# Optimization experiments

Hardware: AMD Instinct MI355X
Metric: run time of the kernel (lower is better)

The kernel has to match this reference:

```python
import jax, jax.numpy as jnp
import numpy as np

F_DIM, H, B, MAX = 128, 256, 256, 128
N = B * MAX            # 32768 nodes, 256 graphs of 128 nodes each
E = 524288             # avg degree 16
EPS = 1e-5


def _bn(x, g, b):
    # BatchNorm1d in training mode: biased batch stats over the node axis
    m = x.mean(0)
    v = x.var(0)
    return (x - m) * jax.lax.rsqrt(v + EPS) * g + b


def _gcn(x, W, b, src, dst, n):
    # PyG GCNConv: add self-loops, symmetric deg^-1/2 normalization
    h = x @ W
    loops = jnp.arange(n, dtype=src.dtype)
    s = jnp.concatenate([src, loops])
    d = jnp.concatenate([dst, loops])
    deg = jax.ops.segment_sum(jnp.ones_like(s, dtype=x.dtype), d, num_segments=n)
    dinv = jax.lax.rsqrt(jnp.maximum(deg, 1.0))
    norm = dinv[s] * dinv[d]
    out = jax.ops.segment_sum(h[s] * norm[:, None], d, num_segments=n)
    return out + b


def setup_inputs() -> dict:
    key = jax.random.key(0)
    ks = jax.random.split(key, 20)

    def xavier(k, shape, gain=1.414):
        lim = gain * np.sqrt(6.0 / (shape[0] + shape[1]))
        return jax.random.uniform(k, shape, jnp.float32, -lim, lim)

    inp = {}
    inp['x'] = jax.random.normal(ks[0], (N, F_DIM), jnp.float32)
    inp['src_local'] = jax.random.randint(ks[1], (E,), 0, MAX, jnp.int32)
    inp['dst_local'] = jax.random.randint(ks[2], (E,), 0, MAX, jnp.int32)
    dims = [(F_DIM, H), (H, H), (H, H)]
    for i, (di, do) in enumerate(dims):
        inp[f'gcn_w{i}'] = xavier(ks[3 + i], (di, do))
        inp[f'gcn_b{i}'] = jnp.zeros((do,), jnp.float32)
        inp[f'bn_g{i}'] = jnp.ones((do,), jnp.float32)
        inp[f'bn_b{i}'] = jnp.zeros((do,), jnp.float32)
    inp['sc_w0'] = xavier(ks[6], (F_DIM, H), 1.0)
    inp['sc_b0'] = jnp.zeros((H,), jnp.float32)
    inp['edge_w'] = xavier(ks[7], (H, H), 0.01)
    inp['fd_w0'] = xavier(ks[8], (H, H)); inp['fd_b0'] = jnp.zeros((H,), jnp.float32)
    inp['fd_g0'] = jnp.ones((H,), jnp.float32); inp['fd_be0'] = jnp.zeros((H,), jnp.float32)
    inp['fd_w1'] = xavier(ks[9], (H, H)); inp['fd_b1'] = jnp.zeros((H,), jnp.float32)
    inp['fd_g1'] = jnp.ones((H,), jnp.float32); inp['fd_be1'] = jnp.zeros((H,), jnp.float32)
    inp['fd_w2'] = xavier(ks[10], (H, F_DIM)); inp['fd_b2'] = jnp.zeros((F_DIM,), jnp.float32)
    inp['ph_w0'] = xavier(ks[11], (H, H)); inp['ph_b0'] = jnp.zeros((H,), jnp.float32)
    inp['ph_w1'] = xavier(ks[12], (H, H)); inp['ph_b1'] = jnp.zeros((H,), jnp.float32)
    return inp


def reference(x, src_local, dst_local,
              gcn_w0, gcn_b0, bn_g0, bn_b0, sc_w0, sc_b0,
              gcn_w1, gcn_b1, bn_g1, bn_b1,
              gcn_w2, gcn_b2, bn_g2, bn_b2,
              edge_w,
              fd_w0, fd_b0, fd_g0, fd_be0,
              fd_w1, fd_b1, fd_g1, fd_be1,
              fd_w2, fd_b2,
              ph_w0, ph_b0, ph_w1, ph_b1):
    n = x.shape[0]
    # global edge index: edge e belongs to graph e // (E//B); offset by g*MAX
    off = (jnp.arange(E, dtype=jnp.int32) // (E // B)) * MAX
    src = src_local + off
    dst = dst_local + off

    def block(h, W, b, g, bb, shortcut):
        res = shortcut(h)
        out = jax.nn.relu(_bn(_gcn(h, W, b, src, dst, n), g, bb))
        return jax.nn.relu(out + res)  # dropout is identity at inference

    z = block(x, gcn_w0, gcn_b0, bn_g0, bn_b0, lambda h: h @ sc_w0 + sc_b0)
    z = block(z, gcn_w1, gcn_b1, bn_g1, bn_b1, lambda h: h)
    z = block(z, gcn_w2, gcn_b2, bn_g2, bn_b2, lambda h: h)
    # F.normalize(p=2, dim=1)
    z = z / jnp.maximum(jnp.linalg.norm(z, axis=1, keepdims=True), 1e-12)

    # BilinearEdgeDecoder per graph, vectorized: sigmoid(Z W Z^T) with zero diag
    zb = z.reshape(B, MAX, H)
    adj = jax.nn.sigmoid(jnp.einsum('bnd,de,bme->bnm', zb, edge_w, zb))
    adj = adj * (1.0 - jnp.eye(MAX, dtype=adj.dtype))

    # Feature_Decoder: [Linear,ReLU,BN] x2 then Linear
    h = _bn(jax.nn.relu(z @ fd_w0 + fd_b0), fd_g0, fd_be0)
    h = _bn(jax.nn.relu(h @ fd_w1 + fd_b1), fd_g1, fd_be1)
    x_recon = h @ fd_w2 + fd_b2

    z_g = zb.max(axis=1)  # global_max_pool per graph
    z_g_mlp = jax.nn.relu(z_g @ ph_w0 + ph_b0) @ ph_w1 + ph_b1
    return (z, adj, x_recon, z_g, z_g_mlp)
```

## Files before the change

kernel.cpp:

```cpp
#include <hip/hip_runtime.h>
#include <hip/hip_bf16.h>

using bf = __hip_bfloat16;
typedef __attribute__((ext_vector_type(8))) short s8;
typedef __attribute__((ext_vector_type(4))) float f4;

constexpr int NN  = 32768;
constexpr int HD  = 256;

__device__ __forceinline__ float u2f(unsigned short h) {
    union { unsigned u; float f; } x; x.u = ((unsigned)h) << 16;
    return x.f;
}
__device__ __forceinline__ unsigned short f2u(float f) {
    union { float f; unsigned u; } x; x.f = f;
    unsigned r = x.u + 0x7FFF + ((x.u >> 16) & 1);
    return (unsigned short)(r >> 16);
}
__device__ __forceinline__ bf f2bf(float f) {
    unsigned short h = f2u(f);
    return *reinterpret_cast<bf*>(&h);
}
__device__ __forceinline__ float bf2f(bf b) {
    return u2f(*reinterpret_cast<unsigned short*>(&b));
}

__device__ __forceinline__ int swz(int row, int slot) {
    return row * 64 + ((slot ^ (row & 7)) << 3);
}
__device__ __forceinline__ int swz128(int row, int slot) {
    return row * 128 + ((slot ^ (row & 7)) << 3);
}

typedef const __attribute__((address_space(1))) unsigned int guint;
typedef __attribute__((address_space(3))) unsigned int luint;
__device__ __forceinline__ void gload16(const void* g, void* l) {
    __builtin_amdgcn_global_load_lds((guint*)g, (luint*)l, 16, 0, 0);
}

struct WTd { const float* src; int K, N, off; };
struct WTpack { WTd w[10]; };

__global__ __launch_bounds__(256) void k_prep(const int* __restrict__ srcL,
                                              const int* __restrict__ dstL,
                                              const float* __restrict__ xf,
                                              WTpack p, bf* __restrict__ A,
                                              bf* __restrict__ xb,
                                              bf* __restrict__ wT) {
    __shared__ __align__(16) float shm[8320];
    int b = blockIdx.x, t = threadIdx.x;
    if (b < 256) {
        float* sT = shm;
        float* sdin = shm + 8192;
        int g = b;
        const int* sg = srcL + (g << 11);
        const int* dg = dstL + (g << 11);
        if (t < 128) sdin[t] = 0.f;
        __syncthreads();
        for (int e = t; e < 2048; e += 256) atomicAdd(&sdin[dg[e]], 1.0f);
        __syncthreads();
        if (t < 128) sdin[t] = rsqrtf(sdin[t] + 1.0f);
        __syncthreads();
        bf* out = A + ((long)g << 14);
        for (int half = 0; half < 2; ++half) {
            for (int i = t; i < 8192; i += 256) sT[i] = 0.f;
            __syncthreads();
            for (int e = t; e < 2048; e += 256) {
                int s = sg[e], d = dg[e];
                if ((s >> 6) == half)
                    atomicAdd(&sT[(d << 6) + (s & 63)], sdin[s] * sdin[d]);
            }
            __syncthreads();
            if (t < 128 && (t >> 6) == half)
                sT[(t << 6) + (t & 63)] += sdin[t] * sdin[t];
            __syncthreads();
            for (int i4 = t; i4 < 2048; i4 += 256) {
                int d = i4 >> 4, c4 = (i4 & 15) * 4;
                float4 v = *(float4*)&sT[(d << 6) + c4];
                ushort4 u = make_ushort4(f2u(v.x), f2u(v.y), f2u(v.z), f2u(v.w));
                *(ushort4*)&out[(d << 7) + (half << 6) + c4] = u;
            }
            __syncthreads();
        }
    } else if (b < 416) {
        int idx = b - 256;
        WTd d = p.w[idx >> 4];
        int rem = idx & 15;
        int n0 = (rem & 3) * 64, k0 = (rem >> 2) * 64;
        if (n0 >= d.N || k0 >= d.K) return;
        float (*s)[65] = (float(*)[65])shm;
        int cc = t & 63, rq = t >> 6;
#pragma unroll
        for (int i = 0; i < 16; ++i) {
            int r = i * 4 + rq;
            s[r][cc] = d.src[(long)(k0 + r) * d.N + n0 + cc];
        }
        __syncthreads();
#pragma unroll
        for (int i = 0; i < 16; ++i) {
            int r = i * 4 + rq;
            wT[d.off + (long)(n0 + r) * d.K + k0 + cc] = f2bf(s[cc][r]);
        }
    } else {
        long base = (long)(b - 416) * 16384;
#pragma unroll
        for (int it = 0; it < 16; ++it) {
            long i4 = base + (it * 256 + t) * 4;
            float4 v = *(const float4*)&xf[i4];
            *(ushort4*)&xb[i4] = make_ushort4(f2u(v.x), f2u(v.y), f2u(v.z), f2u(v.w));
        }
    }
}

__device__ __forceinline__ void mfma_s1(const bf* sA, const bf* sB, f4 (&acc)[4][2],
                                        int wm, int wn, int l15, int kq) {
#pragma unroll
    for (int ks = 0; ks < 2; ++ks) {
        s8 af[4], bg[2];
#pragma unroll
        for (int f = 0; f < 4; ++f)
            af[f] = *(const s8*)&sA[swz(wm * 64 + f * 16 + l15, kq + 4 * ks)];
#pragma unroll
        for (int f = 0; f < 2; ++f)
            bg[f] = *(const s8*)&sB[swz(wn * 32 + f * 16 + l15, kq + 4 * ks)];
#pragma unroll
        for (int fr = 0; fr < 4; ++fr)
#pragma unroll
            for (int fc = 0; fc < 2; ++fc)
                acc[fr][fc] = __builtin_amdgcn_mfma_f32_16x16x32_bf16(
                    af[fr], bg[fc], acc[fr][fc], 0, 0, 0);
    }
}

__device__ __forceinline__ void mfma_s2(const bf* sA, const bf* sB, f4 (&acc)[4][2],
                                        int wm, int wn, int l15, int kq) {
#pragma unroll
    for (int ks = 0; ks < 4; ++ks) {
        s8 af[4], bg[2];
#pragma unroll
        for (int f = 0; f < 4; ++f)
            af[f] = *(const s8*)&sA[swz128(wm * 64 + f * 16 + l15, ks * 4 + kq)];
#pragma unroll
        for (int f = 0; f < 2; ++f)
            bg[f] = *(const s8*)&sB[swz128(wn * 32 + f * 16 + l15, ks * 4 + kq)];
#pragma unroll
        for (int fr = 0; fr < 4; ++fr)
#pragma unroll
            for (int fc = 0; fc < 2; ++fc)
                acc[fr][fc] = __builtin_amdgcn_mfma_f32_16x16x32_bf16(
                    af[fr], bg[fc], acc[fr][fc], 0, 0, 0);
    }
}

__device__ __forceinline__ void tstore(bf* sOut, f4 (&acc)[4][2],
                                       int wm, int wn, int l15, int kq) {
#pragma unroll
    for (int fr = 0; fr < 4; ++fr) {
        int rl = wm * 64 + fr * 16 + kq * 4;
#pragma unroll
        for (int fc = 0; fc < 2; ++fc) {
            int cl = wn * 32 + fc * 16 + l15;
            ushort4 q = make_ushort4(f2u(acc[fr][fc][0]), f2u(acc[fr][fc][1]),
                                     f2u(acc[fr][fc][2]), f2u(acc[fr][fc][3]));
            int off = cl * 128 + (((rl >> 3) ^ (cl & 7)) << 3) + (rl & 7);
            *(ushort4*)&sOut[off] = q;
        }
    }
}

template <int MODE>
__global__ __launch_bounds__(512) void k_fused(
    const bf* __restrict__ Xin,
    const bf* __restrict__ Res, const float* __restrict__ stats,
    const bf* __restrict__ Wt, const bf* __restrict__ Wt2,
    const float* __restrict__ scb, const bf* __restrict__ Adj,
    bf* __restrict__ Zout, bf* __restrict__ AG, bf* __restrict__ ResOut,
    float* __restrict__ part) {
    __shared__ __align__(16) bf sOut[16384];
    __shared__ __align__(16) bf sStg[16384];
    const int g = blockIdx.x;
    const int h = blockIdx.y;
    const int t = threadIdx.x;
    const int lane = t & 63, w = t >> 6;
    const int wm = w >> 2, wn = w & 3;
    const int l15 = lane & 15, kq = lane >> 4;
    constexpr int KS1 = (MODE == 2) ? 128 : 256;
    const bf* Xg = Xin + (long)g * ((MODE == 2) ? 16384 : 32768);
    const bf* Rg = (MODE == 0) ? Res + (long)g * 32768 : nullptr;

    f4 acc1[4][2] = {};
    for (int k0 = 0; k0 < KS1; k0 += 64) {
        __syncthreads();
#pragma unroll
        for (int i = 0; i < 2; ++i) {
            if constexpr (MODE == 0) {
                int sdx = i * 512 + t;
                int row = sdx >> 3, sl = sdx & 7;
                int c = k0 + sl * 8;
                s8 av = *(const s8*)&Xg[row * 256 + c];
                s8 rv = *(const s8*)&Rg[row * 256 + c];
                float4 sc0 = *(const float4*)&stats[c];
                float4 sc1 = *(const float4*)&stats[c + 4];
                float4 sh0 = *(const float4*)&stats[256 + c];
                float4 sh1 = *(const float4*)&stats[256 + c + 4];
                float scv[8] = {sc0.x, sc0.y, sc0.z, sc0.w, sc1.x, sc1.y, sc1.z, sc1.w};
                float shv[8] = {sh0.x, sh0.y, sh0.z, sh0.w, sh1.x, sh1.y, sh1.z, sh1.w};
                unsigned short* u = (unsigned short*)&av;
                const unsigned short* ru = (const unsigned short*)&rv;
#pragma unroll
                for (int j = 0; j < 8; ++j) {
                    float v = fmaf(u2f(u[j]), scv[j], shv[j]);
                    v = fmaxf(v, 0.f) + u2f(ru[j]);
                    u[j] = f2u(fmaxf(v, 0.f));
                }
                if (h == 0)
                    *(s8*)&Zout[(long)g * 32768 + row * 256 + c] = av;
                *(s8*)&sStg[swz(row, sl)] = av;
            } else {
                int r0 = i * 64 + 8 * w;
                int rw = r0 + (lane >> 3);
                int ps = ((lane & 7) ^ (rw & 7)) << 3;
                gload16(&Xg[rw * 128 + k0 + ps], &sStg[r0 * 64]);
            }
            {
                int r0 = i * 64 + 8 * w;
                int rw = r0 + (lane >> 3);
                int ps = ((lane & 7) ^ (rw & 7)) << 3;
                const bf* bsrc;
                if constexpr (MODE == 0)
                    bsrc = &Wt[(h * 128 + rw) * 256 + k0 + ps];
                else {
                    const bf* Wsrc = (h < 2) ? Wt : Wt2;
                    bsrc = &Wsrc[((h & 1) * 128 + rw) * 128 + k0 + ps];
                }
                gload16(bsrc, &sStg[8192 + r0 * 64]);
            }
        }
        __syncthreads();
        mfma_s1(sStg, sStg + 8192, acc1, wm, wn, l15, kq);
    }
    if (MODE == 2 && h >= 2) {
#pragma unroll
        for (int fr = 0; fr < 4; ++fr) {
            int rl = wm * 64 + fr * 16 + kq * 4;
#pragma unroll
            for (int fc = 0; fc < 2; ++fc) {
                int cl = wn * 32 + fc * 16 + l15;
                float bv = scb[(h - 2) * 128 + cl];
#pragma unroll
                for (int i = 0; i < 4; ++i)
                    ResOut[(long)(g * 128 + rl + i) * 256 + (h - 2) * 128 + cl] =
                        f2bf(acc1[fr][fc][i] + bv);
            }
        }
        return;
    }
    tstore(sOut, acc1, wm, wn, l15, kq);
    __syncthreads();
#pragma unroll
    for (int i = 0; i < 4; ++i) {
        int r0 = i * 32 + 4 * w;
        int rw = r0 + (lane >> 4);
        int ps = ((lane & 15) ^ (rw & 7)) << 3;
        gload16(&Adj[((long)g << 14) + rw * 128 + ps], &sStg[r0 * 128]);
    }
    __syncthreads();
    f4 acc2[4][2] = {};
    mfma_s2(sStg, sOut, acc2, wm, wn, l15, kq);
    float ps[2] = {0.f, 0.f}, ps2[2] = {0.f, 0.f};
#pragma unroll
    for (int fr = 0; fr < 4; ++fr) {
        int rl = wm * 64 + fr * 16 + kq * 4;
#pragma unroll
        for (int fc = 0; fc < 2; ++fc) {
            int cl = wn * 32 + fc * 16 + l15;
#pragma unroll
            for (int i = 0; i < 4; ++i) {
                float v = acc2[fr][fc][i];
                ps[fc] += v; ps2[fc] += v * v;
                AG[(long)(g * 128 + rl + i) * 256 + (h & 1) * 128 + cl] = f2bf(v);
            }
        }
    }
    __syncthreads();
    float* scr = (float*)sStg;
#pragma unroll
    for (int fc = 0; fc < 2; ++fc) {
        ps[fc] += __shfl_xor(ps[fc], 16);  ps[fc] += __shfl_xor(ps[fc], 32);
        ps2[fc] += __shfl_xor(ps2[fc], 16); ps2[fc] += __shfl_xor(ps2[fc], 32);
    }
    if (lane < 16) {
#pragma unroll
        for (int fc = 0; fc < 2; ++fc) {
            int c = wn * 32 + fc * 16 + lane;
            scr[(c * 2 + wm) * 2 + 0] = ps[fc];
            scr[(c * 2 + wm) * 2 + 1] = ps2[fc];
        }
    }
    __syncthreads();
    if (t < 256) {
        int col = t & 127, s = t >> 7;
        part[(long)((h & 1) * 256 + g) * 256 + s * 128 + col] =
            scr[(col * 2 + 0) * 2 + s] + scr[(col * 2 + 1) * 2 + s];
    }
}

__device__ __forceinline__ void fd_layer(const bf* Zg, const bf* W, const float* bias,
                                         bf* C, float* part, bf* sStg,
                                         int g, int h, int t, int lane,
                                         int wm, int wn, int l15, int kq) {
    f4 acc[4][2] = {};
    for (int k0 = 0; k0 < 256; k0 += 64) {
        __syncthreads();
#pragma unroll
        for (int i = 0; i < 2; ++i) {
            int sdx = i * 512 + t;
            int row = sdx >> 3, sl = sdx & 7;
            int c = k0 + sl * 8;
            *(s8*)&sStg[swz(row, sl)] = *(const s8*)&Zg[row * 256 + c];
            *(s8*)&sStg[8192 + swz(row, sl)] = *(const s8*)&W[(h * 128 + row) * 256 + c];
        }
        __syncthreads();
        mfma_s1(sStg, sStg + 8192, acc, wm, wn, l15, kq);
    }
    float ps[2] = {0.f, 0.f}, ps2[2] = {0.f, 0.f};
#pragma unroll
    for (int fr = 0; fr < 4; ++fr) {
        int rl = wm * 64 + fr * 16 + kq * 4;
#pragma unroll
        for (int fc = 0; fc < 2; ++fc) {
            int cl = wn * 32 + fc * 16 + l15;
            float bv = bias[h * 128 + cl];
#pragma unroll
            for (int i = 0; i < 4; ++i) {
                float v = fmaxf(acc[fr][fc][i] + bv, 0.f);
                ps[fc] += v; ps2[fc] += v * v;
                C[(long)(g * 128 + rl + i) * 256 + h * 128 + cl] = f2bf(v);
            }
        }
    }
    __syncthreads();
    float* scr = (float*)sStg;
#pragma unroll
    for (int fc = 0; fc < 2; ++fc) {
        ps[fc] += __shfl_xor(ps[fc], 16);  ps[fc] += __shfl_xor(ps[fc], 32);
        ps2[fc] += __shfl_xor(ps2[fc], 16); ps2[fc] += __shfl_xor(ps2[fc], 32);
    }
    if (lane < 16) {
#pragma unroll
        for (int fc = 0; fc < 2; ++fc) {
            int c = wn * 32 + fc * 16 + lane;
            scr[(c * 2 + wm) * 2 + 0] = ps[fc];
            scr[(c * 2 + wm) * 2 + 1] = ps2[fc];
        }
    }
    __syncthreads();
    if (t < 256) {
        int col = t & 127, s = t >> 7;
        part[(long)(h * 256 + g) * 256 + s * 128 + col] =
            scr[(col * 2 + 0) * 2 + s] + scr[(col * 2 + 1) * 2 + s];
    }
}

__global__ __launch_bounds__(512) void k_edfd(
    const bf* __restrict__ Zn, const bf* __restrict__ ewT,
    const bf* __restrict__ fdw, const float* __restrict__ fdb,
    float* __restrict__ adjout, bf* __restrict__ C, float* __restrict__ part) {
    __shared__ __align__(16) bf sOut[16384];
    __shared__ __align__(16) bf sStg[16384];
    const int t = threadIdx.x;
    const int lane = t & 63, w = t >> 6;
    const int wm = w >> 2, wn = w & 3;
    const int l15 = lane & 15, kq = lane >> 4;
    if (blockIdx.x >= 256) {
        int bb = blockIdx.x - 256;
        int g = bb & 255, h = bb >> 8;
        fd_layer(Zn + (long)g * 32768, fdw, fdb, C, part, sStg,
                 g, h, t, lane, wm, wn, l15, kq);
        return;
    }
    const int g = blockIdx.x;
    const bf* Xg = Zn + (long)g * 32768;
    f4 acc2[4][2] = {};
    for (int h = 0; h < 2; ++h) {
        f4 acc1[4][2] = {};
        for (int k0 = 0; k0 < 256; k0 += 64) {
            __syncthreads();
#pragma unroll
            for (int i = 0; i < 2; ++i) {
                int sdx = i * 512 + t;
                int row = sdx >> 3, sl = sdx & 7;
                int c = k0 + sl * 8;
                *(s8*)&sStg[swz(row, sl)] = *(const s8*)&ewT[(h * 128 + row) * 256 + c];
                *(s8*)&sStg[8192 + swz(row, sl)] = *(const s8*)&Xg[row * 256 + c];
            }
            __syncthreads();
            mfma_s1(sStg, sStg + 8192, acc1, wm, wn, l15, kq);
        }
        tstore(sOut, acc1, wm, wn, l15, kq);
        __syncthreads();
#pragma unroll
        for (int i = 0; i < 4; ++i) {
            int sdx = i * 512 + t;
            int row = sdx >> 4, sl = sdx & 15;
            *(s8*)&sStg[swz128(row, sl)] = *(const s8*)&Xg[row * 256 + h * 128 + sl * 8];
        }
        __syncthreads();
        mfma_s2(sStg, sOut, acc2, wm, wn, l15, kq);
        __syncthreads();
    }
#pragma unroll
    for (int fr = 0; fr < 4; ++fr) {
        int rl = wm * 64 + fr * 16 + kq * 4;
#pragma unroll
        for (int fc = 0; fc < 2; ++fc) {
            int cl = wn * 32 + fc * 16 + l15;
            float vv[4];
#pragma unroll
            for (int i = 0; i < 4; ++i) {
                float v = 1.f / (1.f + __expf(-acc2[fr][fc][i]));
                if (cl == rl + i) v = 0.f;
                vv[i] = v;
            }
            float4 o; o.x = vv[0]; o.y = vv[1]; o.z = vv[2]; o.w = vv[3];
            *(float4*)&adjout[((long)g << 14) + cl * 128 + rl] = o;
        }
    }
}

template <int EPI, int OUT, bool PART, bool BNA, bool AF32>
__global__ __launch_bounds__(256) void mg(
    const void* __restrict__ Av, const bf* __restrict__ BT,
    const float* __restrict__ bias, const float* __restrict__ bnstats,
    float* __restrict__ Cf, bf* __restrict__ Cb, float* __restrict__ part,
    int M, int N, int K, int ldc) {
    __shared__ __align__(16) bf sAl[128 * 64];
    __shared__ __align__(16) bf sBl[128 * 64];
    const int m0 = blockIdx.y * 128, n0 = blockIdx.x * 128;
    const bf* Bb = BT + (long)n0 * K;
    const int t = threadIdx.x;
    const int lane = t & 63;
    const int w = t >> 6;
    const int wm = (w >> 1) * 64, wn = (w & 1) * 64;
    const int fr16 = lane & 15, kq = lane >> 4;
    f4 acc[4][4] = {};
    for (int k0 = 0; k0 < K; k0 += 64) {
#pragma unroll
        for (int i = 0; i < 4; ++i) {
            int sdx = i * 256 + t;
            int row = sdx >> 3, sl = sdx & 7;
            s8 av;
            if constexpr (AF32) {
                const float* src = (const float*)Av + (long)(m0 + row) * K + k0 + sl * 8;
                float4 f0 = *(const float4*)src;
                float4 f1 = *(const float4*)(src + 4);
                unsigned short u[8] = {f2u(f0.x), f2u(f0.y), f2u(f0.z), f2u(f0.w),
                                       f2u(f1.x), f2u(f1.y), f2u(f1.z), f2u(f1.w)};
                av = *(s8*)u;
            } else {
                av = *(const s8*)&((const bf*)Av)[(long)(m0 + row) * K + k0 + sl * 8];
                if constexpr (BNA) {
                    int c = k0 + sl * 8;
                    float4 sc0 = *(const float4*)&bnstats[c];
                    float4 sc1 = *(const float4*)&bnstats[c + 4];
                    float4 sh0 = *(const float4*)&bnstats[256 + c];
                    float4 sh1 = *(const float4*)&bnstats[256 + c + 4];
                    float scv[8] = {sc0.x, sc0.y, sc0.z, sc0.w, sc1.x, sc1.y, sc1.z, sc1.w};
                    float shv[8] = {sh0.x, sh0.y, sh0.z, sh0.w, sh1.x, sh1.y, sh1.z, sh1.w};
                    unsigned short* u = (unsigned short*)&av;
#pragma unroll
                    for (int j = 0; j < 8; ++j)
                        u[j] = f2u(fmaf(u2f(u[j]), scv[j], shv[j]));
                }
            }
            *(s8*)&sAl[swz(row, sl)] = av;
            *(s8*)&sBl[swz(row, sl)] = *(const s8*)&Bb[(long)row * K + k0 + sl * 8];
        }
        __syncthreads();
#pragma unroll
        for (int ks = 0; ks < 2; ++ks) {
            s8 af[4], bg[4];
#pragma unroll
            for (int f = 0; f < 4; ++f) {
                af[f] = *(const s8*)&sAl[swz(wm + f * 16 + fr16, kq + 4 * ks)];
                bg[f] = *(const s8*)&sBl[swz(wn + f * 16 + fr16, kq + 4 * ks)];
            }
#pragma unroll
            for (int fr = 0; fr < 4; ++fr)
#pragma unroll
                for (int fc = 0; fc < 4; ++fc)
                    acc[fr][fc] = __builtin_amdgcn_mfma_f32_16x16x32_bf16(
                        af[fr], bg[fc], acc[fr][fc], 0, 0, 0);
        }
        __syncthreads();
    }
    float ps[4], ps2[4];
    if (PART) {
#pragma unroll
        for (int fc = 0; fc < 4; ++fc) { ps[fc] = 0.f; ps2[fc] = 0.f; }
    }
#pragma unroll
    for (int fr = 0; fr < 4; ++fr) {
        int rl = wm + fr * 16 + (lane >> 4) * 4;
#pragma unroll
        for (int fc = 0; fc < 4; ++fc) {
            int cl = wn + fc * 16 + (lane & 15);
            int col = n0 + cl;
            float bv = bias[col];
#pragma unroll
            for (int i = 0; i < 4; ++i) {
                float v = acc[fr][fc][i] + bv;
                if (EPI == 2) v = fmaxf(v, 0.f);
                if (PART) { ps[fc] += v; ps2[fc] += v * v; }
                if (OUT == 0) Cf[(long)(m0 + rl + i) * ldc + col] = v;
                if (OUT == 1) Cb[(long)(m0 + rl + i) * ldc + col] = f2bf(v);
            }
        }
    }
    if (PART) {
        __syncthreads();
        float* scr = (float*)sAl;
#pragma unroll
        for (int fc = 0; fc < 4; ++fc) {
            ps[fc] += __shfl_xor(ps[fc], 16);  ps[fc] += __shfl_xor(ps[fc], 32);
            ps2[fc] += __shfl_xor(ps2[fc], 16); ps2[fc] += __shfl_xor(ps2[fc], 32);
        }
        if (lane < 16) {
#pragma unroll
            for (int fc = 0; fc < 4; ++fc) {
                scr[(w * 2 + 0) * 64 + fc * 16 + lane] = ps[fc];
                scr[(w * 2 + 1) * 64 + fc * 16 + lane] = ps2[fc];
            }
        }
        __syncthreads();
        int id = blockIdx.x * gridDim.y + blockIdx.y;
        int stat = t >> 7, c = t & 127;
        int ci = c & 63, half = c >> 6;
        float v = scr[(half * 2 + stat) * 64 + ci] + scr[((half + 2) * 2 + stat) * 64 + ci];
        part[(long)id * 256 + stat * 128 + c] = v;
    }
}

__global__ void k_bnfin(const float* __restrict__ part, const float* __restrict__ gam,
                        const float* __restrict__ bet, float* __restrict__ stats) {
    int ch = blockIdx.x;
    int half = ch >> 7, cc = ch & 127;
    int t = threadIdx.x;
    __shared__ float2 sm[256];
    const float* p = part + (long)(half * 256 + t) * 256;
    sm[t] = make_float2(p[cc], p[128 + cc]);
    __syncthreads();
    for (int s = 128; s > 0; s >>= 1) {
        if (t < s) { sm[t].x += sm[t + s].x; sm[t].y += sm[t + s].y; }
        __syncthreads();
    }
    if (t == 0) {
        float m = sm[0].x / (float)NN;
        float var = sm[0].y / (float)NN - m * m;
        float sc = rsqrtf(var + 1e-5f) * gam[ch];
        stats[ch]       = sc;
        stats[256 + ch] = bet[ch] - m * sc;
    }
}

__global__ __launch_bounds__(512) void k_finz(
    const bf* __restrict__ X, const float* __restrict__ stats,
    const bf* __restrict__ res, float* __restrict__ outz, bf* __restrict__ Znb,
    unsigned* __restrict__ zgu) {
    int g = blockIdx.x, half = blockIdx.y;
    int t = threadIdx.x;
    int lane = t & 63, w = t >> 6;
    int c4 = lane * 4;
    float4 sc = *(const float4*)&stats[c4];
    float4 sh = *(const float4*)&stats[256 + c4];
    float scv[4] = {sc.x, sc.y, sc.z, sc.w};
    float shv[4] = {sh.x, sh.y, sh.z, sh.w};
    float cmax[4] = {0.f, 0.f, 0.f, 0.f};
#pragma unroll
    for (int it = 0; it < 8; ++it) {
        int r = half * 64 + w * 8 + it;
        long i = (long)(g * 128 + r) * 256 + c4;
        ushort4 xv = *(const ushort4*)(X + i);
        ushort4 rv = *(const ushort4*)(res + i);
        unsigned short xs[4] = {xv.x, xv.y, xv.z, xv.w};
        unsigned short rs[4] = {rv.x, rv.y, rv.z, rv.w};
        float v[4];
        float s = 0.f;
#pragma unroll
        for (int j = 0; j < 4; ++j) {
            float vv = fmaf(u2f(xs[j]), scv[j], shv[j]);
            vv = fmaxf(vv, 0.f) + u2f(rs[j]);
            vv = fmaxf(vv, 0.f);
            v[j] = vv;
            s += vv * vv;
        }
#pragma unroll
        for (int o = 1; o < 64; o <<= 1) s += __shfl_xor(s, o);
        float den = fmaxf(sqrtf(s), 1e-12f);
        float4 fo;
        unsigned short us[4];
#pragma unroll
        for (int j = 0; j < 4; ++j) {
            float o = v[j] / den;
            ((float*)&fo)[j] = o;
            us[j] = f2u(o);
            cmax[j] = fmaxf(cmax[j], o);
        }
        *(float4*)(outz + i) = fo;
        *(ushort4*)(Znb + i) = make_ushort4(us[0], us[1], us[2], us[3]);
    }
    __shared__ float pm[8][256];
#pragma unroll
    for (int j = 0; j < 4; ++j) pm[w][c4 + j] = cmax[j];
    __syncthreads();
    if (t < 256) {
        float m = pm[0][t];
#pragma unroll
        for (int ww = 1; ww < 8; ++ww) m = fmaxf(m, pm[ww][t]);
        atomicMax(&zgu[g * 256 + t], __float_as_uint(m));
    }
}

template <int EPI, int OUT, bool PART, bool BNA, bool AF32>
static void MG(hipStream_t st, const void* A, const bf* BT, const float* bias,
               const float* bnstats, float* Cf, bf* Cb, float* part,
               int M, int N, int K, int ldc) {
    dim3 g(N / 128, M / 128, 1);
    mg<EPI, OUT, PART, BNA, AF32><<<g, 256, 0, st>>>(A, BT, bias, bnstats, Cf, Cb, part,
                                                     M, N, K, ldc);
}

extern "C" void kernel_launch(void* const* d_in, const int* in_sizes, int n_in,
                              void* d_out, int out_size, void* d_ws, size_t ws_size,
                              hipStream_t stream) {
    const float* x      = (const float*)d_in[0];
    const int*   srcL   = (const int*)d_in[1];
    const int*   dstL   = (const int*)d_in[2];
    const float* gcn_w0 = (const float*)d_in[3];
    const float* bn_g0  = (const float*)d_in[5];
    const float* bn_b0  = (const float*)d_in[6];
    const float* gcn_w1 = (const float*)d_in[7];
    const float* bn_g1  = (const float*)d_in[9];
    const float* bn_b1  = (const float*)d_in[10];
    const float* gcn_w2 = (const float*)d_in[11];
    const float* bn_g2  = (const float*)d_in[13];
    const float* bn_b2  = (const float*)d_in[14];
    const float* sc_w0  = (const float*)d_in[15];
    const float* sc_b0  = (const float*)d_in[16];
    const float* edge_w = (const float*)d_in[17];
    const float* fd_w0  = (const float*)d_in[18];
    const float* fd_b0  = (const float*)d_in[19];
    const float* fd_g0  = (const float*)d_in[20];
    const float* fd_be0 = (const float*)d_in[21];
    const float* fd_w1  = (const float*)d_in[22];
    const float* fd_b1  = (const float*)d_in[23];
    const float* fd_g1  = (const float*)d_in[24];
    const float* fd_be1 = (const float*)d_in[25];
    const float* fd_w2  = (const float*)d_in[26];
    const float* fd_b2  = (const float*)d_in[27];
    const float* ph_w0  = (const float*)d_in[28];
    const float* ph_b0  = (const float*)d_in[29];
    const float* ph_w1  = (const float*)d_in[30];
    const float* ph_b1  = (const float*)d_in[31];

    float* out     = (float*)d_out;
    float* out_z   = out;
    float* out_adj = out + 8388608;
    float* out_xr  = out + 12582912;
    float* out_zg  = out + 16777216;
    float* out_zgm = out + 16842752;

    float* w     = (float*)d_ws;
    float* part  = w;
    float* stats = w + 131072;
    bf*    wT    = (bf*)(w + 131584);
    bf*    Aadjb = (bf*)(w + 410112);
    bf*    U4    = (bf*)(w + 2507264);
    bf*    U1    = (bf*)(w + 6701568);
    bf*    U2    = (bf*)(w + 10895872);
    bf*    U3    = (bf*)(w + 15090176);
    bf*    P1b   = (bf*)(w + 19284480);
    bf*    xb    = (bf*)(w + 19317248);

    WTpack pk;
    pk.w[0] = {gcn_w0, 128, 256, 0};
    pk.w[1] = {sc_w0,  128, 256, 32768};
    pk.w[2] = {gcn_w1, 256, 256, 65536};
    pk.w[3] = {gcn_w2, 256, 256, 131072};
    pk.w[4] = {edge_w, 256, 256, 196608};
    pk.w[5] = {fd_w0,  256, 256, 262144};
    pk.w[6] = {fd_w1,  256, 256, 327680};
    pk.w[7] = {fd_w2,  256, 128, 393216};
    pk.w[8] = {ph_w0,  256, 256, 425984};
    pk.w[9] = {ph_w1,  256, 256, 491520};

    hipMemsetAsync(out_zg, 0, 65536 * 4, stream);

    k_prep<<<672, 256, 0, stream>>>(srcL, dstL, x, pk, Aadjb, xb, wT);

    k_fused<2><<<dim3(256, 4), 512, 0, stream>>>(xb, nullptr, nullptr,
                                                 wT + 0, wT + 32768, sc_b0, Aadjb,
                                                 nullptr, U2, U1, part);
    k_bnfin<<<256, 256, 0, stream>>>(part, bn_g0, bn_b0, stats);

    k_fused<0><<<dim3(256, 2), 512, 0, stream>>>(U2, U1, stats,
                                                 wT + 65536, nullptr, nullptr, Aadjb,
                                                 U3, U4, nullptr, part);
    k_bnfin<<<256, 256, 0, stream>>>(part, bn_g1, bn_b1, stats);

    k_fused<0><<<dim3(256, 2), 512, 0, stream>>>(U4, U3, stats,
                                                 wT + 131072, nullptr, nullptr, Aadjb,
                                                 U1, U2, nullptr, part);
    k_bnfin<<<256, 256, 0, stream>>>(part, bn_g2, bn_b2, stats);

    k_finz<<<dim3(256, 2), 512, 0, stream>>>(U2, stats, U1, out_z, U3,
                                             (unsigned*)out_zg);

    k_edfd<<<768, 512, 0, stream>>>(U3, wT + 196608, wT + 262144, fd_b0,
                                    out_adj, U4, part);
    k_bnfin<<<256, 256, 0, stream>>>(part, fd_g0, fd_be0, stats);

    MG<2, 1, true, true, false>(stream, U4, wT + 327680, fd_b1, stats,
                                nullptr, U2, part, NN, HD, HD, 256);
    k_bnfin<<<256, 256, 0, stream>>>(part, fd_g1, fd_be1, stats);
    MG<1, 0, false, true, false>(stream, U2, wT + 393216, fd_b2, stats,
                                 out_xr, nullptr, nullptr, NN, 128, HD, 128);

    MG<2, 1, false, false, true>(stream, out_zg, wT + 425984, ph_b0, nullptr,
                                 nullptr, P1b, nullptr, 256, 256, 256, 256);
    MG<1, 0, false, false, false>(stream, P1b, wT + 491520, ph_b1, nullptr,
                                  out_zgm, nullptr, nullptr, 256, 256, 256, 256);
}
```

Baseline: 182.8 us.

## Fuse GCN trunk layers, BN finalize and normalize into one cooperative kernel

Replaces the chain of three fused GCN kernels, three BN-finalize kernels and the final normalize/max-pool kernel with a single persistent cooperative kernel of 512 blocks. Grid-wide syncs separate the layers, and the BN statistics reduction is done inline by half the blocks. The aim is to remove several kernel launch gaps and tail effects. In exchange it adds grid-sync overhead. Each layer-0 block now runs the GCN and shortcut GEMMs back to back. Operand staging changes from direct global-to-LDS loads to loads through registers. A fallback path keeps the multi-kernel sequence in case the cooperative launch fails.

```diff
diff --git a/kernel.cpp b/kernel.cpp
--- a/kernel.cpp
+++ b/kernel.cpp
@@ -1,5 +1,8 @@
 #include <hip/hip_runtime.h>
 #include <hip/hip_bf16.h>
+#include <hip/hip_cooperative_groups.h>
+
+namespace cg = cooperative_groups;
 
 using bf = __hip_bfloat16;
 typedef __attribute__((ext_vector_type(8))) short s8;
@@ -30,12 +33,6 @@
 }
 __device__ __forceinline__ int swz128(int row, int slot) {
     return row * 128 + ((slot ^ (row & 7)) << 3);
-}
-
-typedef const __attribute__((address_space(1))) unsigned int guint;
-typedef __attribute__((address_space(3))) unsigned int luint;
-__device__ __forceinline__ void gload16(const void* g, void* l) {
-    __builtin_amdgcn_global_load_lds((guint*)g, (luint*)l, 16, 0, 0);
 }
 
 struct WTd { const float* src; int K, N, off; };
@@ -168,141 +165,355 @@
     }
 }
 
-template <int MODE>
-__global__ __launch_bounds__(512) void k_fused(
-    const bf* __restrict__ Xin,
-    const bf* __restrict__ Res, const float* __restrict__ stats,
-    const bf* __restrict__ Wt, const bf* __restrict__ Wt2,
-    const float* __restrict__ scb, const bf* __restrict__ Adj,
-    bf* __restrict__ Zout, bf* __restrict__ AG, bf* __restrict__ ResOut,
-    float* __restrict__ part) {
+__device__ __forceinline__ void stageAdj(bf* sStg, const bf* Adj, int g, int t) {
+#pragma unroll
+    for (int i = 0; i < 4; ++i) {
+        int sdx = i * 512 + t;
+        int row = sdx >> 4, sl = sdx & 15;
+        *(s8*)&sStg[swz128(row, sl)] =
+            *(const s8*)&Adj[((long)g << 14) + row * 128 + sl * 8];
+    }
+}
+
+__device__ __forceinline__ void ag_part(f4 (&acc2)[4][2], bf* AG, float* part,
+                                        bf* sStg, int g, int h, int t,
+                                        int wm, int wn, int l15, int kq, int lane) {
+    float ps[2] = {0.f, 0.f}, ps2[2] = {0.f, 0.f};
+#pragma unroll
+    for (int fr = 0; fr < 4; ++fr) {
+        int rl = wm * 64 + fr * 16 + kq * 4;
+#pragma unroll
+        for (int fc = 0; fc < 2; ++fc) {
+            int cl = wn * 32 + fc * 16 + l15;
+#pragma unroll
+            for (int i = 0; i < 4; ++i) {
+                float v = acc2[fr][fc][i];
+                ps[fc] += v; ps2[fc] += v * v;
+                AG[(long)(g * 128 + rl + i) * 256 + h * 128 + cl] = f2bf(v);
+            }
+        }
+    }
+    __syncthreads();
+    float* scr = (float*)sStg;
+#pragma unroll
+    for (int fc = 0; fc < 2; ++fc) {
+        ps[fc] += __shfl_xor(ps[fc], 16);  ps[fc] += __shfl_xor(ps[fc], 32);
+        ps2[fc] += __shfl_xor(ps2[fc], 16); ps2[fc] += __shfl_xor(ps2[fc], 32);
+    }
+    if (lane < 16) {
+#pragma unroll
+        for (int fc = 0; fc < 2; ++fc) {
+            int c = wn * 32 + fc * 16 + lane;
+            scr[(c * 2 + wm) * 2 + 0] = ps[fc];
+            scr[(c * 2 + wm) * 2 + 1] = ps2[fc];
+        }
+    }
+    __syncthreads();
+    if (t < 256) {
+        int col = t & 127, s = t >> 7;
+        part[(long)(h * 256 + g) * 256 + s * 128 + col] =
+            scr[(col * 2 + 0) * 2 + s] + scr[(col * 2 + 1) * 2 + s];
+    }
+}
+
+__device__ __forceinline__ void gcn_layer(const bf* Xg, const bf* Rg,
+                                          const float* stats, const bf* W,
+                                          const bf* Adj, bf* Zout, bf* AG,
+                                          float* part, bf* sOut, bf* sStg,
+                                          int g, int h, int t, int lane,
+                                          int wm, int wn, int l15, int kq) {
+    f4 acc1[4][2] = {};
+    for (int k0 = 0; k0 < 256; k0 += 64) {
+        __syncthreads();
+#pragma unroll
+        for (int i = 0; i < 2; ++i) {
+            int sdx = i * 512 + t;
+            int row = sdx >> 3, sl = sdx & 7;
+            int c = k0 + sl * 8;
+            s8 av = *(const s8*)&Xg[row * 256 + c];
+            s8 rv = *(const s8*)&Rg[row * 256 + c];
+            float4 sc0 = *(const float4*)&stats[c];
+            float4 sc1 = *(const float4*)&stats[c + 4];
+            float4 sh0 = *(const float4*)&stats[256 + c];
+            float4 sh1 = *(const float4*)&stats[256 + c + 4];
+            float scv[8] = {sc0.x, sc0.y, sc0.z, sc0.w, sc1.x, sc1.y, sc1.z, sc1.w};
+            float shv[8] = {sh0.x, sh0.y, sh0.z, sh0.w, sh1.x, sh1.y, sh1.z, sh1.w};
+            unsigned short* u = (unsigned short*)&av;
+            const unsigned short* ru = (const unsigned short*)&rv;
+#pragma unroll
+            for (int j = 0; j < 8; ++j) {
+                float v = fmaf(u2f(u[j]), scv[j], shv[j]);
+                v = fmaxf(v, 0.f) + u2f(ru[j]);
+                u[j] = f2u(fmaxf(v, 0.f));
+            }
+            if (Zout) *(s8*)&Zout[(long)g * 32768 + row * 256 + c] = av;
+            *(s8*)&sStg[swz(row, sl)] = av;
+            *(s8*)&sStg[8192 + swz(row, sl)] = *(const s8*)&W[(h * 128 + row) * 256 + c];
+        }
+        __syncthreads();
+        mfma_s1(sStg, sStg + 8192, acc1, wm, wn, l15, kq);
+    }
+    tstore(sOut, acc1, wm, wn, l15, kq);
+    __syncthreads();
+    stageAdj(sStg, Adj, g, t);
+    __syncthreads();
+    f4 acc2[4][2] = {};
+    mfma_s2(sStg, sOut, acc2, wm, wn, l15, kq);
+    ag_part(acc2, AG, part, sStg, g, h, t, wm, wn, l15, kq, lane);
+}
+
+__device__ __forceinline__ void l0_gcn(const bf* Xg, const bf* W0, const bf* Adj,
+                                       bf* AG, float* part, bf* sOut, bf* sStg,
+                                       int g, int h, int t, int lane,
+                                       int wm, int wn, int l15, int kq) {
+    f4 acc1[4][2] = {};
+    for (int k0 = 0; k0 < 128; k0 += 64) {
+        __syncthreads();
+#pragma unroll
+        for (int i = 0; i < 2; ++i) {
+            int sdx = i * 512 + t;
+            int row = sdx >> 3, sl = sdx & 7;
+            int c = k0 + sl * 8;
+            *(s8*)&sStg[swz(row, sl)] = *(const s8*)&Xg[row * 128 + c];
+            *(s8*)&sStg[8192 + swz(row, sl)] = *(const s8*)&W0[(h * 128 + row) * 128 + c];
+        }
+        __syncthreads();
+        mfma_s1(sStg, sStg + 8192, acc1, wm, wn, l15, kq);
+    }
+    tstore(sOut, acc1, wm, wn, l15, kq);
+    __syncthreads();
+    stageAdj(sStg, Adj, g, t);
+    __syncthreads();
+    f4 acc2[4][2] = {};
+    mfma_s2(sStg, sOut, acc2, wm, wn, l15, kq);
+    ag_part(acc2, AG, part, sStg, g, h, t, wm, wn, l15, kq, lane);
+}
+
+__device__ __forceinline__ void l0_sc(const bf* Xg, const bf* Wsc, const float* scb,
+                                      bf* ResOut, bf* sStg, int g, int h, int t,
+                                      int wm, int wn, int l15, int kq) {
+    f4 acc1[4][2] = {};
+    for (int k0 = 0; k0 < 128; k0 += 64) {
+        __syncthreads();
+#pragma unroll
+        for (int i = 0; i < 2; ++i) {
+            int sdx = i * 512 + t;
+            int row = sdx >> 3, sl = sdx & 7;
+            int c = k0 + sl * 8;
+            *(s8*)&sStg[swz(row, sl)] = *(const s8*)&Xg[row * 128 + c];
+            *(s8*)&sStg[8192 + swz(row, sl)] = *(const s8*)&Wsc[(h * 128 + row) * 128 + c];
+        }
+        __syncthreads();
+        mfma_s1(sStg, sStg + 8192, acc1, wm, wn, l15, kq);
+    }
+#pragma unroll
+    for (int fr = 0; fr < 4; ++fr) {
+        int rl = wm * 64 + fr * 16 + kq * 4;
+#pragma unroll
+        for (int fc = 0; fc < 2; ++fc) {
+            int cl = wn * 32 + fc * 16 + l15;
+            float bv = scb[h * 128 + cl];
+#pragma unroll
+            for (int i = 0; i < 4; ++i)
+                ResOut[(long)(g * 128 + rl + i) * 256 + h * 128 + cl] =
+                    f2bf(acc1[fr][fc][i] + bv);
+        }
+    }
+}
+
+__device__ __forceinline__ void bnfin_inline(const float* part, const float* gam,
+                                             const float* bet, float* stats,
+                                             void* lds, int ch, int t) {
+    float2* sm = (float2*)lds;
+    int half = ch >> 7, cc = ch & 127;
+    if (t < 256) {
+        const float* p = part + (long)(half * 256 + t) * 256;
+        sm[t] = make_float2(p[cc], p[128 + cc]);
+    }
+    __syncthreads();
+    for (int s = 128; s > 0; s >>= 1) {
+        if (t < s) { sm[t].x += sm[t + s].x; sm[t].y += sm[t + s].y; }
+        __syncthreads();
+    }
+    if (t == 0) {
+        float m = sm[0].x / (float)NN;
+        float var = sm[0].y / (float)NN - m * m;
+        float sc = rsqrtf(var + 1e-5f) * gam[ch];
+        stats[ch]       = sc;
+        stats[256 + ch] = bet[ch] - m * sc;
+    }
+}
+
+__device__ __forceinline__ void finz_inline(const bf* X, const float* stats,
+                                            const bf* res, float* outz, bf* Znb,
+                                            unsigned* zgu, float* pmLds,
+                                            int g, int half, int t) {
+    int lane = t & 63, w = t >> 6;
+    int c4 = lane * 4;
+    float4 sc = *(const float4*)&stats[c4];
+    float4 sh = *(const float4*)&stats[256 + c4];
+    float scv[4] = {sc.x, sc.y, sc.z, sc.w};
+    float shv[4] = {sh.x, sh.y, sh.z, sh.w};
+    float cmax[4] = {0.f, 0.f, 0.f, 0.f};
+#pragma unroll
+    for (int it = 0; it < 8; ++it) {
+        int r = half * 64 + w * 8 + it;
+        long i = (long)(g * 128 + r) * 256 + c4;
+        ushort4 xv = *(const ushort4*)(X + i);
+        ushort4 rv = *(const ushort4*)(res + i);
+        unsigned short xs[4] = {xv.x, xv.y, xv.z, xv.w};
+        unsigned short rs[4] = {rv.x, rv.y, rv.z, rv.w};
+        float v[4];
+        float s = 0.f;
+#pragma unroll
+        for (int j = 0; j < 4; ++j) {
+            float vv = fmaf(u2f(xs[j]), scv[j], shv[j]);
+            vv = fmaxf(vv, 0.f) + u2f(rs[j]);
+            vv = fmaxf(vv, 0.f);
+            v[j] = vv;
+            s += vv * vv;
+        }
+#pragma unroll
+        for (int o = 1; o < 64; o <<= 1) s += __shfl_xor(s, o);
+        float den = fmaxf(sqrtf(s), 1e-12f);
+        float4 fo;
+        unsigned short us[4];
+#pragma unroll
+        for (int j = 0; j < 4; ++j) {
+            float o = v[j] / den;
+            ((float*)&fo)[j] = o;
+            us[j] = f2u(o);
+            cmax[j] = fmaxf(cmax[j], o);
+        }
+        *(float4*)(outz + i) = fo;
+        *(ushort4*)(Znb + i) = make_ushort4(us[0], us[1], us[2], us[3]);
+    }
+    float (*pm)[256] = (float(*)[256])pmLds;
+    __syncthreads();
+#pragma unroll
+    for (int j = 0; j < 4; ++j) pm[w][c4 + j] = cmax[j];
+    __syncthreads();
+    if (t < 256) {
+        float m = pm[0][t];
+#pragma unroll
+        for (int ww = 1; ww < 8; ++ww) m = fmaxf(m, pm[ww][t]);
+        atomicMax(&zgu[g * 256 + t], __float_as_uint(m));
+    }
+}
+
+struct TrunkArgs {
+    const bf* xb; const bf* Adj; const bf* wT;
+    const float* scb;
+    const float* g0; const float* be0;
+    const float* g1; const float* be1;
+    const float* g2; const float* be2;
+    bf* U1; bf* U2; bf* U3; bf* U4;
+    float* part; float* stats;
+    float* outz; unsigned* zgu;
+};
+
+__global__ __launch_bounds__(512, 4) void k_trunk(TrunkArgs a) {
     __shared__ __align__(16) bf sOut[16384];
     __shared__ __align__(16) bf sStg[16384];
-    const int g = blockIdx.x;
-    const int h = blockIdx.y;
+    cg::grid_group gg = cg::this_grid();
+    const int b = blockIdx.x;
+    const int g = b & 255, hs = b >> 8;
     const int t = threadIdx.x;
     const int lane = t & 63, w = t >> 6;
     const int wm = w >> 2, wn = w & 3;
     const int l15 = lane & 15, kq = lane >> 4;
-    constexpr int KS1 = (MODE == 2) ? 128 : 256;
-    const bf* Xg = Xin + (long)g * ((MODE == 2) ? 16384 : 32768);
-    const bf* Rg = (MODE == 0) ? Res + (long)g * 32768 : nullptr;
-
-    f4 acc1[4][2] = {};
-    for (int k0 = 0; k0 < KS1; k0 += 64) {
-        __syncthreads();
-#pragma unroll
-        for (int i = 0; i < 2; ++i) {
-            if constexpr (MODE == 0) {
-                int sdx = i * 512 + t;
-                int row = sdx >> 3, sl = sdx & 7;
-                int c = k0 + sl * 8;
-                s8 av = *(const s8*)&Xg[row * 256 + c];
-                s8 rv = *(const s8*)&Rg[row * 256 + c];
-                float4 sc0 = *(const float4*)&stats[c];
-                float4 sc1 = *(const float4*)&stats[c + 4];
-                float4 sh0 = *(const float4*)&stats[256 + c];
-                float4 sh1 = *(const float4*)&stats[256 + c + 4];
-                float scv[8] = {sc0.x, sc0.y, sc0.z, sc0.w, sc1.x, sc1.y, sc1.z, sc1.w};
-                float shv[8] = {sh0.x, sh0.y, sh0.z, sh0.w, sh1.x, sh1.y, sh1.z, sh1.w};
-                unsigned short* u = (unsigned short*)&av;
-                const unsigned short* ru = (const unsigned short*)&rv;
-#pragma unroll
-                for (int j = 0; j < 8; ++j) {
-                    float v = fmaf(u2f(u[j]), scv[j], shv[j]);
-                    v = fmaxf(v, 0.f) + u2f(ru[j]);
-                    u[j] = f2u(fmaxf(v, 0.f));
-                }
-                if (h == 0)
-                    *(s8*)&Zout[(long)g * 32768 + row * 256 + c] = av;
-                *(s8*)&sStg[swz(row, sl)] = av;
-            } else {
-                int r0 = i * 64 + 8 * w;
-                int rw = r0 + (lane >> 3);
-                int ps = ((lane & 7) ^ (rw & 7)) << 3;
-                gload16(&Xg[rw * 128 + k0 + ps], &sStg[r0 * 64]);
-            }
-            {
-                int r0 = i * 64 + 8 * w;
-                int rw = r0 + (lane >> 3);
-                int ps = ((lane & 7) ^ (rw & 7)) << 3;
-                const bf* bsrc;
-                if constexpr (MODE == 0)
-                    bsrc = &Wt[(h * 128 + rw) * 256 + k0 + ps];
-                else {
-                    const bf* Wsrc = (h < 2) ? Wt : Wt2;
-                    bsrc = &Wsrc[((h & 1) * 128 + rw) * 128 + k0 + ps];
-                }
-                gload16(bsrc, &sStg[8192 + r0 * 64]);
-            }
-        }
-        __syncthreads();
-        mfma_s1(sStg, sStg + 8192, acc1, wm, wn, l15, kq);
-    }
-    if (MODE == 2 && h >= 2) {
-#pragma unroll
-        for (int fr = 0; fr < 4; ++fr) {
-            int rl = wm * 64 + fr * 16 + kq * 4;
-#pragma unroll
-            for (int fc = 0; fc < 2; ++fc) {
-                int cl = wn * 32 + fc * 16 + l15;
-                float bv = scb[(h - 2) * 128 + cl];
-#pragma unroll
-                for (int i = 0; i < 4; ++i)
-                    ResOut[(long)(g * 128 + rl + i) * 256 + (h - 2) * 128 + cl] =
-                        f2bf(acc1[fr][fc][i] + bv);
-            }
-        }
-        return;
-    }
-    tstore(sOut, acc1, wm, wn, l15, kq);
-    __syncthreads();
-#pragma unroll
-    for (int i = 0; i < 4; ++i) {
-        int r0 = i * 32 + 4 * w;
-        int rw = r0 + (lane >> 4);
-        int ps = ((lane & 15) ^ (rw & 7)) << 3;
-        gload16(&Adj[((long)g << 14) + rw * 128 + ps], &sStg[r0 * 128]);
-    }
-    __syncthreads();
-    f4 acc2[4][2] = {};
-    mfma_s2(sStg, sOut, acc2, wm, wn, l15, kq);
-    float ps[2] = {0.f, 0.f}, ps2[2] = {0.f, 0.f};
-#pragma unroll
-    for (int fr = 0; fr < 4; ++fr) {
-        int rl = wm * 64 + fr * 16 + kq * 4;
-#pragma unroll
-        for (int fc = 0; fc < 2; ++fc) {
-            int cl = wn * 32 + fc * 16 + l15;
-#pragma unroll
-            for (int i = 0; i < 4; ++i) {
-                float v = acc2[fr][fc][i];
-                ps[fc] += v; ps2[fc] += v * v;
-                AG[(long)(g * 128 + rl + i) * 256 + (h & 1) * 128 + cl] = f2bf(v);
-            }
-        }
-    }
-    __syncthreads();
-    float* scr = (float*)sStg;
-#pragma unroll
-    for (int fc = 0; fc < 2; ++fc) {
-        ps[fc] += __shfl_xor(ps[fc], 16);  ps[fc] += __shfl_xor(ps[fc], 32);
-        ps2[fc] += __shfl_xor(ps2[fc], 16); ps2[fc] += __shfl_xor(ps2[fc], 32);
-    }
-    if (lane < 16) {
-#pragma unroll
-        for (int fc = 0; fc < 2; ++fc) {
-            int c = wn * 32 + fc * 16 + lane;
-            scr[(c * 2 + wm) * 2 + 0] = ps[fc];
-            scr[(c * 2 + wm) * 2 + 1] = ps2[fc];
-        }
-    }
-    __syncthreads();
-    if (t < 256) {
-        int col = t & 127, s = t >> 7;
-        part[(long)((h & 1) * 256 + g) * 256 + s * 128 + col] =
-            scr[(col * 2 + 0) * 2 + s] + scr[(col * 2 + 1) * 2 + s];
-    }
+
+    {
+        const bf* Xg = a.xb + (long)g * 16384;
+        l0_gcn(Xg, a.wT, a.Adj, a.U2, a.part, sOut, sStg,
+               g, hs, t, lane, wm, wn, l15, kq);
+        l0_sc(Xg, a.wT + 32768, a.scb, a.U1, sStg, g, hs, t, wm, wn, l15, kq);
+    }
+    gg.sync();
+    if (hs == 0) bnfin_inline(a.part, a.g0, a.be0, a.stats, sStg, g, t);
+    gg.sync();
+
+    gcn_layer(a.U2 + (long)g * 32768, a.U1 + (long)g * 32768, a.stats,
+              a.wT + 65536, a.Adj, hs == 0 ? a.U3 : nullptr, a.U4, a.part,
+              sOut, sStg, g, hs, t, lane, wm, wn, l15, kq);
+    gg.sync();
+    if (hs == 0) bnfin_inline(a.part, a.g1, a.be1, a.stats, sStg, g, t);
+    gg.sync();
+
+    gcn_layer(a.U4 + (long)g * 32768, a.U3 + (long)g * 32768, a.stats,
+              a.wT + 131072, a.Adj, hs == 0 ? a.U1 : nullptr, a.U2, a.part,
+              sOut, sStg, g, hs, t, lane, wm, wn, l15, kq);
+    gg.sync();
+    if (hs == 0) bnfin_inline(a.part, a.g2, a.be2, a.stats, sStg, g, t);
+    gg.sync();
+
+    finz_inline(a.U2, a.stats, a.U1, a.outz, a.U3, a.zgu, (float*)sStg, g, hs, t);
+}
+
+__global__ __launch_bounds__(512) void k_fall0(
+    const bf* __restrict__ xb, const bf* __restrict__ W0, const bf* __restrict__ Wsc,
+    const float* __restrict__ scb, const bf* __restrict__ Adj,
+    bf* __restrict__ AG, bf* __restrict__ ResOut, float* __restrict__ part) {
+    __shared__ __align__(16) bf sOut[16384];
+    __shared__ __align__(16) bf sStg[16384];
+    const int g = blockIdx.x, h = blockIdx.y;
+    const int t = threadIdx.x;
+    const int lane = t & 63, w = t >> 6;
+    const int wm = w >> 2, wn = w & 3;
+    const int l15 = lane & 15, kq = lane >> 4;
+    const bf* Xg = xb + (long)g * 16384;
+    if (h < 2)
+        l0_gcn(Xg, W0, Adj, AG, part, sOut, sStg, g, h, t, lane, wm, wn, l15, kq);
+    else
+        l0_sc(Xg, Wsc, scb, ResOut, sStg, g, h - 2, t, wm, wn, l15, kq);
+}
+
+__global__ __launch_bounds__(512) void k_fall(
+    const bf* __restrict__ Xin, const bf* __restrict__ Res,
+    const float* __restrict__ stats, const bf* __restrict__ Wt,
+    const bf* __restrict__ Adj, bf* __restrict__ Zout, bf* __restrict__ AG,
+    float* __restrict__ part) {
+    __shared__ __align__(16) bf sOut[16384];
+    __shared__ __align__(16) bf sStg[16384];
+    const int g = blockIdx.x, h = blockIdx.y;
+    const int t = threadIdx.x;
+    const int lane = t & 63, w = t >> 6;
+    const int wm = w >> 2, wn = w & 3;
+    const int l15 = lane & 15, kq = lane >> 4;
+    gcn_layer(Xin + (long)g * 32768, Res + (long)g * 32768, stats, Wt, Adj,
+              h == 0 ? Zout : nullptr, AG, part, sOut, sStg,
+              g, h, t, lane, wm, wn, l15, kq);
+}
+
+__global__ void k_bnfin(const float* __restrict__ part, const float* __restrict__ gam,
+                        const float* __restrict__ bet, float* __restrict__ stats) {
+    int ch = blockIdx.x;
+    int half = ch >> 7, cc = ch & 127;
+    int t = threadIdx.x;
+    __shared__ float2 sm[256];
+    const float* p = part + (long)(half * 256 + t) * 256;
+    sm[t] = make_float2(p[cc], p[128 + cc]);
+    __syncthreads();
+    for (int s = 128; s > 0; s >>= 1) {
+        if (t < s) { sm[t].x += sm[t + s].x; sm[t].y += sm[t + s].y; }
+        __syncthreads();
+    }
+    if (t == 0) {
+        float m = sm[0].x / (float)NN;
+        float var = sm[0].y / (float)NN - m * m;
+        float sc = rsqrtf(var + 1e-5f) * gam[ch];
+        stats[ch]       = sc;
+        stats[256 + ch] = bet[ch] - m * sc;
+    }
+}
+
+__global__ __launch_bounds__(512) void k_finz(
+    const bf* __restrict__ X, const float* __restrict__ stats,
+    const bf* __restrict__ res, float* __restrict__ outz, bf* __restrict__ Znb,
+    unsigned* __restrict__ zgu) {
+    __shared__ float pm[8][256];
+    finz_inline(X, stats, res, outz, Znb, zgu, (float*)pm,
+                blockIdx.x, blockIdx.y, threadIdx.x);
 }
 
 __device__ __forceinline__ void fd_layer(const bf* Zg, const bf* W, const float* bias,
@@ -538,86 +749,6 @@
         int ci = c & 63, half = c >> 6;
         float v = scr[(half * 2 + stat) * 64 + ci] + scr[((half + 2) * 2 + stat) * 64 + ci];
         part[(long)id * 256 + stat * 128 + c] = v;
-    }
-}
-
-__global__ void k_bnfin(const float* __restrict__ part, const float* __restrict__ gam,
-                        const float* __restrict__ bet, float* __restrict__ stats) {
-    int ch = blockIdx.x;
-    int half = ch >> 7, cc = ch & 127;
-    int t = threadIdx.x;
-    __shared__ float2 sm[256];
-    const float* p = part + (long)(half * 256 + t) * 256;
-    sm[t] = make_float2(p[cc], p[128 + cc]);
-    __syncthreads();
-    for (int s = 128; s > 0; s >>= 1) {
-        if (t < s) { sm[t].x += sm[t + s].x; sm[t].y += sm[t + s].y; }
-        __syncthreads();
-    }
-    if (t == 0) {
-        float m = sm[0].x / (float)NN;
-        float var = sm[0].y / (float)NN - m * m;
-        float sc = rsqrtf(var + 1e-5f) * gam[ch];
-        stats[ch]       = sc;
-        stats[256 + ch] = bet[ch] - m * sc;
-    }
-}
-
-__global__ __launch_bounds__(512) void k_finz(
-    const bf* __restrict__ X, const float* __restrict__ stats,
-    const bf* __restrict__ res, float* __restrict__ outz, bf* __restrict__ Znb,
-    unsigned* __restrict__ zgu) {
-    int g = blockIdx.x, half = blockIdx.y;
-    int t = threadIdx.x;
-    int lane = t & 63, w = t >> 6;
-    int c4 = lane * 4;
-    float4 sc = *(const float4*)&stats[c4];
-    float4 sh = *(const float4*)&stats[256 + c4];
-    float scv[4] = {sc.x, sc.y, sc.z, sc.w};
-    float shv[4] = {sh.x, sh.y, sh.z, sh.w};
-    float cmax[4] = {0.f, 0.f, 0.f, 0.f};
-#pragma unroll
-    for (int it = 0; it < 8; ++it) {
-        int r = half * 64 + w * 8 + it;
-        long i = (long)(g * 128 + r) * 256 + c4;
-        ushort4 xv = *(const ushort4*)(X + i);
-        ushort4 rv = *(const ushort4*)(res + i);
-        unsigned short xs[4] = {xv.x, xv.y, xv.z, xv.w};
-        unsigned short rs[4] = {rv.x, rv.y, rv.z, rv.w};
-        float v[4];
-        float s = 0.f;
-#pragma unroll
-        for (int j = 0; j < 4; ++j) {
-            float vv = fmaf(u2f(xs[j]), scv[j], shv[j]);
-            vv = fmaxf(vv, 0.f) + u2f(rs[j]);
-            vv = fmaxf(vv, 0.f);
-            v[j] = vv;
-            s += vv * vv;
-        }
-#pragma unroll
-        for (int o = 1; o < 64; o <<= 1) s += __shfl_xor(s, o);
-        float den = fmaxf(sqrtf(s), 1e-12f);
-        float4 fo;
-        unsigned short us[4];
-#pragma unroll
-        for (int j = 0; j < 4; ++j) {
-            float o = v[j] / den;
-            ((float*)&fo)[j] = o;
-            us[j] = f2u(o);
-            cmax[j] = fmaxf(cmax[j], o);
-        }
-        *(float4*)(outz + i) = fo;
-        *(ushort4*)(Znb + i) = make_ushort4(us[0], us[1], us[2], us[3]);
-    }
-    __shared__ float pm[8][256];
-#pragma unroll
-    for (int j = 0; j < 4; ++j) pm[w][c4 + j] = cmax[j];
-    __syncthreads();
-    if (t < 256) {
-        float m = pm[0][t];
-#pragma unroll
-        for (int ww = 1; ww < 8; ++ww) m = fmaxf(m, pm[ww][t]);
-        atomicMax(&zgu[g * 256 + t], __float_as_uint(m));
     }
 }
 
@@ -698,23 +829,31 @@
 
     k_prep<<<672, 256, 0, stream>>>(srcL, dstL, x, pk, Aadjb, xb, wT);
 
-    k_fused<2><<<dim3(256, 4), 512, 0, stream>>>(xb, nullptr, nullptr,
-                                                 wT + 0, wT + 32768, sc_b0, Aadjb,
-                                                 nullptr, U2, U1, part);
-    k_bnfin<<<256, 256, 0, stream>>>(part, bn_g0, bn_b0, stats);
-
-    k_fused<0><<<dim3(256, 2), 512, 0, stream>>>(U2, U1, stats,
-                                                 wT + 65536, nullptr, nullptr, Aadjb,
-                                                 U3, U4, nullptr, part);
-    k_bnfin<<<256, 256, 0, stream>>>(part, bn_g1, bn_b1, stats);
-
-    k_fused<0><<<dim3(256, 2), 512, 0, stream>>>(U4, U3, stats,
-                                                 wT + 131072, nullptr, nullptr, Aadjb,
-                                                 U1, U2, nullptr, part);
-    k_bnfin<<<256, 256, 0, stream>>>(part, bn_g2, bn_b2, stats);
-
-    k_finz<<<dim3(256, 2), 512, 0, stream>>>(U2, stats, U1, out_z, U3,
-                                             (unsigned*)out_zg);
+    TrunkArgs ta;
+    ta.xb = xb; ta.Adj = Aadjb; ta.wT = wT;
+    ta.scb = sc_b0;
+    ta.g0 = bn_g0; ta.be0 = bn_b0;
+    ta.g1 = bn_g1; ta.be1 = bn_b1;
+    ta.g2 = bn_g2; ta.be2 = bn_b2;
+    ta.U1 = U1; ta.U2 = U2; ta.U3 = U3; ta.U4 = U4;
+    ta.part = part; ta.stats = stats;
+    ta.outz = out_z; ta.zgu = (unsigned*)out_zg;
+    void* kargs[] = {&ta};
+    hipError_t rc = hipLaunchCooperativeKernel(reinterpret_cast<void*>(k_trunk),
+                                               dim3(512), dim3(512), kargs, 0, stream);
+    if (rc != hipSuccess) {
+        k_fall0<<<dim3(256, 4), 512, 0, stream>>>(xb, wT, wT + 32768, sc_b0, Aadjb,
+                                                  U2, U1, part);
+        k_bnfin<<<256, 256, 0, stream>>>(part, bn_g0, bn_b0, stats);
+        k_fall<<<dim3(256, 2), 512, 0, stream>>>(U2, U1, stats, wT + 65536, Aadjb,
+                                                 U3, U4, part);
+        k_bnfin<<<256, 256, 0, stream>>>(part, bn_g1, bn_b1, stats);
+        k_fall<<<dim3(256, 2), 512, 0, stream>>>(U4, U3, stats, wT + 131072, Aadjb,
+                                                 U1, U2, part);
+        k_bnfin<<<256, 256, 0, stream>>>(part, bn_g2, bn_b2, stats);
+        k_finz<<<dim3(256, 2), 512, 0, stream>>>(U2, stats, U1, out_z, U3,
+                                                 (unsigned*)out_zg);
+    }
 
     k_edfd<<<768, 512, 0, stream>>>(U3, wT + 196608, wT + 262144, fd_b0,
                                     out_adj, U4, part);
```

After: 585.6 us. 220% more time.
